# Kernel tuning notes

Hardware: AMD Instinct MI355X
Metric: run time of the kernel (lower is better)

## Reference

```python
import jax, jax.numpy as jnp
import numpy as np

N_NODES = 100000
N_EDGES = 1250000
IN_F, HID_F, OUT_F = 64, 64, 32


def setup_inputs() -> dict:
    key = jax.random.key(0)
    ks = jax.random.split(key, 10)

    def xavier(k, fan_in, fan_out):
        std = jnp.sqrt(2.0 / (fan_in + fan_out))  # gain=sqrt(2) for relu -> std*sqrt(2)
        gain = jnp.sqrt(2.0)
        return (gain * std) * jax.random.normal(k, (fan_in, fan_out), dtype=jnp.float32)

    return {
        "feat": jax.random.normal(ks[0], (N_NODES, IN_F), dtype=jnp.float32),
        "efeat": jax.random.normal(ks[1], (N_EDGES, IN_F), dtype=jnp.float32),
        "src": jax.random.randint(ks[2], (N_EDGES,), 0, N_NODES, dtype=jnp.int32),
        "dst": jax.random.randint(ks[3], (N_EDGES,), 0, N_NODES, dtype=jnp.int32),
        "W_vsk": xavier(ks[4], IN_F, HID_F),
        "b_vsk": jnp.zeros((HID_F,), dtype=jnp.float32),
        "W_vrk": xavier(ks[5], IN_F, HID_F),
        "b_vrk": jnp.zeros((HID_F,), dtype=jnp.float32),
        "W_ek": xavier(ks[6], IN_F, HID_F),
        "b_ek": jnp.zeros((HID_F,), dtype=jnp.float32),
        "W1": xavier(ks[7], HID_F, HID_F),
        "b1": jnp.zeros((HID_F,), dtype=jnp.float32),
        "W2": xavier(ks[8], HID_F, OUT_F),
        "b2": jnp.zeros((OUT_F,), dtype=jnp.float32),
    }


def reference(feat, efeat, src, dst, W_vsk, b_vsk, W_vrk, b_vrk, W_ek, b_ek, W1, b1, W2, b2):
    # Layer 0: project on nodes (N x hid), project edge feats (E x hid)
    vsk = feat @ W_vsk + b_vsk   # [N, hid]
    vrk = feat @ W_vrk + b_vrk   # [N, hid]
    ek = efeat @ W_ek + b_ek     # [E, hid]
    # u_add_v: gather src/dst projections onto edges, fused add + activation
    out = jax.nn.relu(vsk[src] + vrk[dst] + ek)  # [E, hid]
    # Remaining dense layers on edges
    out = jax.nn.relu(out @ W1 + b1)             # [E, hid]
    out = jax.nn.relu(out @ W2 + b2)             # [E, out]
    return out
```

## Files before the change

kernel.cpp:

```cpp
#include <hip/hip_runtime.h>

#define N_NODES 100000
#define N_EDGES 1250000

typedef __bf16 bf16x8 __attribute__((ext_vector_type(8)));
typedef __bf16 bf16x4 __attribute__((ext_vector_type(4)));
typedef float  f32x4  __attribute__((ext_vector_type(4)));

#define MFMA16(a, b, c) __builtin_amdgcn_mfma_f32_16x16x32_bf16((a), (b), (c), 0, 0, 0)

__device__ __forceinline__ int swz(int row, int k) {
    return row * 64 + (((k >> 3) ^ (row & 7)) << 3) + (k & 7);
}

__device__ __forceinline__ void stage_rows_bf16(
    const float* __restrict__ srcmat, long row0, int wb, int lane,
    __bf16* sT, long nrows)
{
#pragma unroll
    for (int i = 0; i < 8; ++i) {
        const int f = (i * 64 + lane) * 4;
        const int rl = f >> 6;
        const int k  = f & 63;
        const int r_loc = wb + rl;
        const long r = row0 + r_loc;
        float4 v = {0.f, 0.f, 0.f, 0.f};
        if (r < nrows) v = *(const float4*)&srcmat[(size_t)r * 64 + k];
        bf16x4 pk = { (__bf16)v.x, (__bf16)v.y, (__bf16)v.z, (__bf16)v.w };
        *(bf16x4*)&sT[swz(r_loc, k)] = pk;
    }
}

__device__ __forceinline__ bf16x8 afrag(const __bf16* sT, int row, int ks, int q) {
    return *(const bf16x8*)&sT[swz(row, ks * 32 + q * 8)];
}

__device__ __forceinline__ void conv_frag(const float* __restrict__ W, int N,
                                          __bf16* __restrict__ dst, int tid) {
    const int NT = N / 16;
    const int slots = 2 * NT * 64;
    for (int s = tid; s < slots; s += 256) {
        const int ks = s / (NT * 64);
        const int nt = (s / 64) % NT;
        const int lane = s % 64;
        const int q = lane >> 4, lc = lane & 15;
#pragma unroll
        for (int j = 0; j < 8; ++j) {
            const int k = ks * 32 + q * 8 + j;
            dst[(size_t)s * 8 + j] = (__bf16)W[(size_t)k * N + nt * 16 + lc];
        }
    }
}

__global__ __launch_bounds__(256) void prep_kernel(
    const float* __restrict__ Wv, const float* __restrict__ Wr,
    const float* __restrict__ We, const float* __restrict__ W1,
    const float* __restrict__ W2,
    __bf16* wfv, __bf16* wfr, __bf16* wfe, __bf16* wf1, __bf16* wf2)
{
    const int t = threadIdx.x;
    conv_frag(Wv, 64, wfv, t);
    conv_frag(Wr, 64, wfr, t);
    conv_frag(We, 64, wfe, t);
    conv_frag(W1, 64, wf1, t);
    conv_frag(W2, 32, wf2, t);
}

__global__ __launch_bounds__(256, 4) void node_kernel(
    const float* __restrict__ feat,
    const float* __restrict__ bv, const float* __restrict__ br,
    const __bf16* __restrict__ wfv, const __bf16* __restrict__ wfr,
    __bf16* __restrict__ vskb, __bf16* __restrict__ vrkb)
{
    __shared__ __align__(16) __bf16 sT[128 * 64];
    const int tid = threadIdx.x;
    const int lane = tid & 63, w = tid >> 6;
    const int q = lane >> 4, lc = lane & 15;
    const long n0 = (long)blockIdx.x * 128;
    const int wb = w * 32;

    stage_rows_bf16(feat, n0, wb, lane, sT, (long)N_NODES);

    bf16x8 a[2][2];
#pragma unroll
    for (int mt = 0; mt < 2; ++mt)
#pragma unroll
        for (int ks = 0; ks < 2; ++ks)
            a[mt][ks] = afrag(sT, wb + mt * 16 + lc, ks, q);

    const __bf16* wf[2] = {wfv, wfr};
    const float* bias[2] = {bv, br};
    __bf16* dstp[2] = {vskb, vrkb};

    for (int m = 0; m < 2; ++m) {
        bf16x8 bfr[4][2];
#pragma unroll
        for (int nt = 0; nt < 4; ++nt)
#pragma unroll
            for (int ks = 0; ks < 2; ++ks)
                bfr[nt][ks] = *(const bf16x8*)&wf[m][((size_t)(ks * 4 + nt) * 64 + lane) * 8];

        f32x4 acc[2][4];
#pragma unroll
        for (int mt = 0; mt < 2; ++mt)
#pragma unroll
            for (int nt = 0; nt < 4; ++nt) {
                f32x4 z = {0.f, 0.f, 0.f, 0.f};
                acc[mt][nt] = z;
            }
#pragma unroll
        for (int ks = 0; ks < 2; ++ks)
#pragma unroll
            for (int mt = 0; mt < 2; ++mt)
#pragma unroll
                for (int nt = 0; nt < 4; ++nt)
                    acc[mt][nt] = MFMA16(a[mt][ks], bfr[nt][ks], acc[mt][nt]);

        float bb[4];
#pragma unroll
        for (int nt = 0; nt < 4; ++nt) bb[nt] = bias[m][nt * 16 + lc];

#pragma unroll
        for (int mt = 0; mt < 2; ++mt)
#pragma unroll
            for (int r = 0; r < 4; ++r) {
                const long node = n0 + wb + mt * 16 + q * 4 + r;
                if (node < N_NODES) {
#pragma unroll
                    for (int nt = 0; nt < 4; ++nt)
                        dstp[m][(size_t)node * 64 + nt * 16 + lc] =
                            (__bf16)(acc[mt][nt][r] + bb[nt]);
                }
            }
    }
}

__global__ __launch_bounds__(256, 4) void edge_kernel(
    const float* __restrict__ efeat,
    const int* __restrict__ src, const int* __restrict__ dst,
    const __bf16* __restrict__ vskb, const __bf16* __restrict__ vrkb,
    const __bf16* __restrict__ wfe, const __bf16* __restrict__ wf1,
    const __bf16* __restrict__ wf2,
    const float* __restrict__ bek, const float* __restrict__ b1,
    const float* __restrict__ b2,
    float* __restrict__ out)
{
    __shared__ __align__(16) __bf16 sT[128 * 64];
    const int tid = threadIdx.x;
    const int lane = tid & 63, w = tid >> 6;
    const int q = lane >> 4, lc = lane & 15;
    const long e0 = (long)blockIdx.x * 128;
    const int wb = w * 32;

    stage_rows_bf16(efeat, e0, wb, lane, sT, (long)N_EDGES);

    bf16x8 a[2][2];
#pragma unroll
    for (int mt = 0; mt < 2; ++mt)
#pragma unroll
        for (int ks = 0; ks < 2; ++ks)
            a[mt][ks] = afrag(sT, wb + mt * 16 + lc, ks, q);

    {
        bf16x8 bfr[4][2];
#pragma unroll
        for (int nt = 0; nt < 4; ++nt)
#pragma unroll
            for (int ks = 0; ks < 2; ++ks)
                bfr[nt][ks] = *(const bf16x8*)&wfe[((size_t)(ks * 4 + nt) * 64 + lane) * 8];

        f32x4 acc[2][4];
#pragma unroll
        for (int mt = 0; mt < 2; ++mt)
#pragma unroll
            for (int nt = 0; nt < 4; ++nt) {
                f32x4 z = {0.f, 0.f, 0.f, 0.f};
                acc[mt][nt] = z;
            }
#pragma unroll
        for (int ks = 0; ks < 2; ++ks)
#pragma unroll
            for (int mt = 0; mt < 2; ++mt)
#pragma unroll
                for (int nt = 0; nt < 4; ++nt)
                    acc[mt][nt] = MFMA16(a[mt][ks], bfr[nt][ks], acc[mt][nt]);

        float bb[4];
#pragma unroll
        for (int nt = 0; nt < 4; ++nt) bb[nt] = bek[nt * 16 + lc];

#pragma unroll
        for (int mt = 0; mt < 2; ++mt)
#pragma unroll
            for (int r = 0; r < 4; ++r) {
                const int e_loc = wb + mt * 16 + q * 4 + r;
                const long e = e0 + e_loc;
                const bool valid = e < N_EDGES;
                int si = 0, di = 0;
                if (valid) { si = src[e]; di = dst[e]; }
#pragma unroll
                for (int nt = 0; nt < 4; ++nt) {
                    const int col = nt * 16 + lc;
                    float hv = 0.f;
                    if (valid) {
                        const float gs = (float)vskb[(size_t)si * 64 + col];
                        const float gd = (float)vrkb[(size_t)di * 64 + col];
                        hv = fmaxf(acc[mt][nt][r] + gs + gd + bb[nt], 0.f);
                    }
                    sT[swz(e_loc, col)] = (__bf16)hv;
                }
            }
    }

    {
#pragma unroll
        for (int mt = 0; mt < 2; ++mt)
#pragma unroll
            for (int ks = 0; ks < 2; ++ks)
                a[mt][ks] = afrag(sT, wb + mt * 16 + lc, ks, q);

        bf16x8 bfr[4][2];
#pragma unroll
        for (int nt = 0; nt < 4; ++nt)
#pragma unroll
            for (int ks = 0; ks < 2; ++ks)
                bfr[nt][ks] = *(const bf16x8*)&wf1[((size_t)(ks * 4 + nt) * 64 + lane) * 8];

        f32x4 acc[2][4];
#pragma unroll
        for (int mt = 0; mt < 2; ++mt)
#pragma unroll
            for (int nt = 0; nt < 4; ++nt) {
                f32x4 z = {0.f, 0.f, 0.f, 0.f};
                acc[mt][nt] = z;
            }
#pragma unroll
        for (int ks = 0; ks < 2; ++ks)
#pragma unroll
            for (int mt = 0; mt < 2; ++mt)
#pragma unroll
                for (int nt = 0; nt < 4; ++nt)
                    acc[mt][nt] = MFMA16(a[mt][ks], bfr[nt][ks], acc[mt][nt]);

        float bb[4];
#pragma unroll
        for (int nt = 0; nt < 4; ++nt) bb[nt] = b1[nt * 16 + lc];

#pragma unroll
        for (int mt = 0; mt < 2; ++mt)
#pragma unroll
            for (int r = 0; r < 4; ++r) {
                const int e_loc = wb + mt * 16 + q * 4 + r;
#pragma unroll
                for (int nt = 0; nt < 4; ++nt) {
                    const int col = nt * 16 + lc;
                    const float hv = fmaxf(acc[mt][nt][r] + bb[nt], 0.f);
                    sT[swz(e_loc, col)] = (__bf16)hv;
                }
            }
    }

    {
#pragma unroll
        for (int mt = 0; mt < 2; ++mt)
#pragma unroll
            for (int ks = 0; ks < 2; ++ks)
                a[mt][ks] = afrag(sT, wb + mt * 16 + lc, ks, q);

        bf16x8 bfr[2][2];
#pragma unroll
        for (int nt = 0; nt < 2; ++nt)
#pragma unroll
            for (int ks = 0; ks < 2; ++ks)
                bfr[nt][ks] = *(const bf16x8*)&wf2[((size_t)(ks * 2 + nt) * 64 + lane) * 8];

        f32x4 acc[2][2];
#pragma unroll
        for (int mt = 0; mt < 2; ++mt)
#pragma unroll
            for (int nt = 0; nt < 2; ++nt) {
                f32x4 z = {0.f, 0.f, 0.f, 0.f};
                acc[mt][nt] = z;
            }
#pragma unroll
        for (int ks = 0; ks < 2; ++ks)
#pragma unroll
            for (int mt = 0; mt < 2; ++mt)
#pragma unroll
                for (int nt = 0; nt < 2; ++nt)
                    acc[mt][nt] = MFMA16(a[mt][ks], bfr[nt][ks], acc[mt][nt]);

        float bb[2] = {b2[lc], b2[16 + lc]};

#pragma unroll
        for (int mt = 0; mt < 2; ++mt)
#pragma unroll
            for (int r = 0; r < 4; ++r) {
                const long e = e0 + wb + mt * 16 + q * 4 + r;
                if (e < N_EDGES) {
#pragma unroll
                    for (int nt = 0; nt < 2; ++nt)
                        out[(size_t)e * 32 + nt * 16 + lc] =
                            fmaxf(acc[mt][nt][r] + bb[nt], 0.f);
                }
            }
    }
}

extern "C" void kernel_launch(void* const* d_in, const int* in_sizes, int n_in,
                              void* d_out, int out_size, void* d_ws, size_t ws_size,
                              hipStream_t stream) {
    const float* feat  = (const float*)d_in[0];
    const float* efeat = (const float*)d_in[1];
    const int*   src   = (const int*)d_in[2];
    const int*   dst   = (const int*)d_in[3];
    const float* W_vsk = (const float*)d_in[4];
    const float* b_vsk = (const float*)d_in[5];
    const float* W_vrk = (const float*)d_in[6];
    const float* b_vrk = (const float*)d_in[7];
    const float* W_ek  = (const float*)d_in[8];
    const float* b_ek  = (const float*)d_in[9];
    const float* W1    = (const float*)d_in[10];
    const float* b1    = (const float*)d_in[11];
    const float* W2    = (const float*)d_in[12];
    const float* b2    = (const float*)d_in[13];
    float* out = (float*)d_out;

    __bf16* vskb = (__bf16*)d_ws;
    __bf16* vrkb = vskb + (size_t)N_NODES * 64;
    __bf16* wfv  = vrkb + (size_t)N_NODES * 64;
    __bf16* wfr  = wfv + 4096;
    __bf16* wfe  = wfr + 4096;
    __bf16* wf1  = wfe + 4096;
    __bf16* wf2  = wf1 + 4096;

    prep_kernel<<<1, 256, 0, stream>>>(W_vsk, W_vrk, W_ek, W1, W2,
                                       wfv, wfr, wfe, wf1, wf2);

    const int node_blocks = (N_NODES + 127) / 128;
    node_kernel<<<node_blocks, 256, 0, stream>>>(feat, b_vsk, b_vrk,
                                                 wfv, wfr, vskb, vrkb);

    const int edge_blocks = (N_EDGES + 127) / 128;
    edge_kernel<<<edge_blocks, 256, 0, stream>>>(efeat, src, dst, vskb, vrkb,
                                                 wfe, wf1, wf2,
                                                 b_ek, b1, b2, out);
}
```

Before: 676.5 us.

## Vectorize src/dst gathers into LDS before edge projection epilogue

Moves the per-edge vsk/vrk row gathers out of the MFMA epilogue: each lane now loads 16-byte bf16x8 chunks of the source and destination projection rows at kernel start and stages them in LDS (a new Gs buffer plus the reused sT buffer). The epilogue then reads the gathered values from LDS instead of issuing scalar 2-byte global loads per output element. This replaces many uncoalesced narrow loads with wide ones issued early so their latency overlaps the efeat staging. In exchange it doubles static LDS use per block, which may lower occupancy under the 4-blocks launch bound.

```diff
diff --git a/kernel.cpp b/kernel.cpp
--- a/kernel.cpp
+++ b/kernel.cpp
@@ -146,11 +146,26 @@
     float* __restrict__ out)
 {
     __shared__ __align__(16) __bf16 sT[128 * 64];
+    __shared__ __align__(16) __bf16 Gs[128 * 64];
     const int tid = threadIdx.x;
     const int lane = tid & 63, w = tid >> 6;
     const int q = lane >> 4, lc = lane & 15;
     const long e0 = (long)blockIdx.x * 128;
     const int wb = w * 32;
+    const int jlo = lane >> 3;
+    const int ch  = lane & 7;
+
+    bf16x8 gdreg[4];
+#pragma unroll
+    for (int i = 0; i < 4; ++i) {
+        const int r_loc = wb + i * 8 + jlo;
+        const long e = e0 + r_loc;
+        int si = 0, di = 0;
+        if (e < (long)N_EDGES) { si = src[e]; di = dst[e]; }
+        bf16x8 gs = *(const bf16x8*)&vskb[(size_t)si * 64 + ch * 8];
+        gdreg[i]  = *(const bf16x8*)&vrkb[(size_t)di * 64 + ch * 8];
+        *(bf16x8*)&Gs[swz(r_loc, ch * 8)] = gs;
+    }
 
     stage_rows_bf16(efeat, e0, wb, lane, sT, (long)N_EDGES);
 
@@ -160,6 +175,10 @@
 #pragma unroll
         for (int ks = 0; ks < 2; ++ks)
             a[mt][ks] = afrag(sT, wb + mt * 16 + lc, ks, q);
+
+#pragma unroll
+    for (int i = 0; i < 4; ++i)
+        *(bf16x8*)&sT[swz(wb + i * 8 + jlo, ch * 8)] = gdreg[i];
 
     {
         bf16x8 bfr[4][2];
@@ -194,30 +213,24 @@
 #pragma unroll
             for (int r = 0; r < 4; ++r) {
                 const int e_loc = wb + mt * 16 + q * 4 + r;
-                const long e = e0 + e_loc;
-                const bool valid = e < N_EDGES;
-                int si = 0, di = 0;
-                if (valid) { si = src[e]; di = dst[e]; }
 #pragma unroll
                 for (int nt = 0; nt < 4; ++nt) {
                     const int col = nt * 16 + lc;
-                    float hv = 0.f;
-                    if (valid) {
-                        const float gs = (float)vskb[(size_t)si * 64 + col];
-                        const float gd = (float)vrkb[(size_t)di * 64 + col];
-                        hv = fmaxf(acc[mt][nt][r] + gs + gd + bb[nt], 0.f);
-                    }
-                    sT[swz(e_loc, col)] = (__bf16)hv;
+                    const int idx = swz(e_loc, col);
+                    const float gsum = (float)Gs[idx] + (float)sT[idx];
+                    const float hv = fmaxf(acc[mt][nt][r] + gsum + bb[nt], 0.f);
+                    sT[idx] = (__bf16)hv;
                 }
             }
     }
 
     {
-#pragma unroll
-        for (int mt = 0; mt < 2; ++mt)
-#pragma unroll
-            for (int ks = 0; ks < 2; ++ks)
-                a[mt][ks] = afrag(sT, wb + mt * 16 + lc, ks, q);
+        bf16x8 a2[2][2];
+#pragma unroll
+        for (int mt = 0; mt < 2; ++mt)
+#pragma unroll
+            for (int ks = 0; ks < 2; ++ks)
+                a2[mt][ks] = afrag(sT, wb + mt * 16 + lc, ks, q);
 
         bf16x8 bfr[4][2];
 #pragma unroll
@@ -240,7 +253,7 @@
             for (int mt = 0; mt < 2; ++mt)
 #pragma unroll
                 for (int nt = 0; nt < 4; ++nt)
-                    acc[mt][nt] = MFMA16(a[mt][ks], bfr[nt][ks], acc[mt][nt]);
+                    acc[mt][nt] = MFMA16(a2[mt][ks], bfr[nt][ks], acc[mt][nt]);
 
         float bb[4];
 #pragma unroll
@@ -261,11 +274,12 @@
     }
 
     {
-#pragma unroll
-        for (int mt = 0; mt < 2; ++mt)
-#pragma unroll
-            for (int ks = 0; ks < 2; ++ks)
-                a[mt][ks] = afrag(sT, wb + mt * 16 + lc, ks, q);
+        bf16x8 a3[2][2];
+#pragma unroll
+        for (int mt = 0; mt < 2; ++mt)
+#pragma unroll
+            for (int ks = 0; ks < 2; ++ks)
+                a3[mt][ks] = afrag(sT, wb + mt * 16 + lc, ks, q);
 
         bf16x8 bfr[2][2];
 #pragma unroll
@@ -288,7 +302,7 @@
             for (int mt = 0; mt < 2; ++mt)
 #pragma unroll
                 for (int nt = 0; nt < 2; ++nt)
-                    acc[mt][nt] = MFMA16(a[mt][ks], bfr[nt][ks], acc[mt][nt]);
+                    acc[mt][nt] = MFMA16(a3[mt][ks], bfr[nt][ks], acc[mt][nt]);
 
         float bb[2] = {b2[lc], b2[16 + lc]};
 
```

After: 614.5 us. -9.2%, faster.
